# Performance work log

Measured on AMD Instinct MI355X. Metric: run time of the kernel, lower is better.

## Reference

```python
import jax, jax.numpy as jnp
import numpy as np

SEQ_LEN, HORIZON = 12, 12
B, N, DIN, DOUT, U = 16, 512, 2, 1, 64
NEG = -1e9


def _gat(x, W, a, b, mask):
    # x: (B, N, F_in); W: (F_in, G); a: (2, G); mask: (N, N) bool
    h = jnp.einsum('bnf,fg->bng', x, W)            # (B, N, G)
    src = jnp.einsum('bng,g->bn', h, a[0])         # (B, N)
    dst = jnp.einsum('bng,g->bn', h, a[1])         # (B, N)
    e = jax.nn.leaky_relu(src[:, :, None] + dst[:, None, :], 0.2)  # (B, N, N)
    e = jnp.where(mask[None], e, NEG)
    alpha = jax.nn.softmax(e, axis=-1)
    return jnp.einsum('bij,bjg->big', alpha, h) + b


def _cell(x, h_prev, W_ru, a_ru, b_ru, W_c, a_c, b_c, mask):
    # graph-attention GRU cell: x (B,N,Din), h_prev (B,N,U)
    xh = jnp.concatenate([x, h_prev], axis=-1)
    ru = jax.nn.sigmoid(_gat(xh, W_ru, a_ru, b_ru, mask))   # (B,N,2U)
    r, u = jnp.split(ru, 2, axis=-1)
    xc = jnp.concatenate([x, r * h_prev], axis=-1)
    c = jnp.tanh(_gat(xc, W_c, a_c, b_c, mask))
    return u * h_prev + (1.0 - u) * c


def setup_inputs() -> dict:
    key = jax.random.key(0)
    ks = jax.random.split(key, 16)
    s = 0.05
    inp = {
        'inputs': jax.random.normal(ks[0], (SEQ_LEN, B, N * DIN), jnp.float32),
        'adj': jax.random.uniform(ks[1], (N, N), jnp.float32),
        # encoder GAGRU cell (input_dim = DIN)
        'enc_W_ru': jax.random.normal(ks[2], (DIN + U, 2 * U), jnp.float32) * s,
        'enc_a_ru': jax.random.normal(ks[3], (2, 2 * U), jnp.float32) * s,
        'enc_b_ru': jnp.zeros((2 * U,), jnp.float32),
        'enc_W_c': jax.random.normal(ks[4], (DIN + U, U), jnp.float32) * s,
        'enc_a_c': jax.random.normal(ks[5], (2, U), jnp.float32) * s,
        'enc_b_c': jnp.zeros((U,), jnp.float32),
        # decoder GAGRU cell (input_dim = DOUT)
        'dec_W_ru': jax.random.normal(ks[6], (DOUT + U, 2 * U), jnp.float32) * s,
        'dec_a_ru': jax.random.normal(ks[7], (2, 2 * U), jnp.float32) * s,
        'dec_b_ru': jnp.zeros((2 * U,), jnp.float32),
        'dec_W_c': jax.random.normal(ks[8], (DOUT + U, U), jnp.float32) * s,
        'dec_a_c': jax.random.normal(ks[9], (2, U), jnp.float32) * s,
        'dec_b_c': jnp.zeros((U,), jnp.float32),
        # projection Linear(rnn_units -> output_dim)
        'proj_W': jax.random.normal(ks[10], (U, DOUT), jnp.float32) * s,
        'proj_b': jnp.zeros((DOUT,), jnp.float32),
    }
    return inp


def reference(inputs, adj, enc_W_ru, enc_a_ru, enc_b_ru, enc_W_c, enc_a_c, enc_b_c,
              dec_W_ru, dec_a_ru, dec_b_ru, dec_W_c, dec_a_c, dec_b_c, proj_W, proj_b):
    mask = (adj > 0.9) | jnp.eye(N, dtype=bool)
    x_seq = inputs.reshape(SEQ_LEN, B, N, DIN)

    # ---- encoder: scan GAGRU cell over seq_len ----
    def enc_step(h, x_t):
        h_new = _cell(x_t, h, enc_W_ru, enc_a_ru, enc_b_ru, enc_W_c, enc_a_c, enc_b_c, mask)
        return h_new, None

    h0 = jnp.zeros((B, N, U), inputs.dtype)
    h_enc, _ = jax.lax.scan(enc_step, h0, x_seq)

    def dec_step(carry, _):
        y_prev, h = carry
        h_new = _cell(y_prev, h, dec_W_ru, dec_a_ru, dec_b_ru, dec_W_c, dec_a_c, dec_b_c, mask)
        y = jnp.einsum('bnu,ud->bnd', h_new, proj_W) + proj_b  # (B, N, DOUT)
        return (y, h_new), y

    go = jnp.zeros((B, N, DOUT), inputs.dtype)
    _, outputs = jax.lax.scan(dec_step, (go, h_enc), None, length=HORIZON)
    return outputs  # (horizon, B, N, DOUT)
```

## Files before the change

kernel.cpp:

```cpp
#include <hip/hip_runtime.h>
#include <math.h>


#define NB 16
#define NN 512
#define NU 64
#define CAP 128
#define WPB 8

#define AS1 __attribute__((address_space(1)))
#define AS3 __attribute__((address_space(3)))

__device__ __forceinline__ void ld_lds16(float* lds_uniform, const float* g_perlane) {
#if __has_builtin(__builtin_amdgcn_global_load_lds)
  __builtin_amdgcn_global_load_lds((const AS1 unsigned int*)g_perlane,
                                   (AS3 unsigned int*)lds_uniform, 16, 0, 0);
#else
  int lane = threadIdx.x & 63;
  *(float4*)(lds_uniform + lane * 4) = *(const float4*)(g_perlane);
#endif
}

__device__ __forceinline__ void stage_weights(float* sW, const float* W, int TB,
                                              int w, int lane) {
  for (int c = w; c * 1024 < TB; c += WPB) {
    int off = c * 1024 + lane * 16;
    if (off < TB)
      ld_lds16((float*)((char*)sW + c * 1024), (const float*)((const char*)W + off));
  }
}

__device__ __forceinline__ float rlane(float v, int l) {
  return __int_as_float(__builtin_amdgcn_readlane(__float_as_int(v), l));
}
__device__ __forceinline__ int rlane_i(int v, int l) {
  return __builtin_amdgcn_readlane(v, l);
}
__device__ __forceinline__ float wave_max(float v) {
  #pragma unroll
  for (int s = 1; s < 64; s <<= 1) v = fmaxf(v, __shfl_xor(v, s));
  return v;
}
__device__ __forceinline__ float wave_sum(float v) {
  #pragma unroll
  for (int s = 1; s < 64; s <<= 1) v += __shfl_xor(v, s);
  return v;
}
__device__ __forceinline__ void wave_sum2(float& x, float& y) {
  #pragma unroll
  for (int s = 1; s < 64; s <<= 1) { x += __shfl_xor(x, s); y += __shfl_xor(y, s); }
}
__device__ __forceinline__ float fast_rcp(float x) {
#if __has_builtin(__builtin_amdgcn_rcpf)
  return __builtin_amdgcn_rcpf(x);
#else
  return 1.0f / x;
#endif
}
__device__ __forceinline__ float sigmoid_f(float x) {
  return fast_rcp(1.0f + __expf(-x));
}
__device__ __forceinline__ float tanh_f(float x) {
  return 1.0f - 2.0f * fast_rcp(__expf(2.0f * x) + 1.0f);
}

__global__ __launch_bounds__(64) void k_adj(const float* __restrict__ adj,
                                            int* __restrict__ cnt,
                                            int* __restrict__ idx) {
  int i = blockIdx.x;
  int l = threadIdx.x;
  int base = 0;
  #pragma unroll
  for (int c = 0; c < 8; ++c) {
    int j = c * 64 + l;
    bool pred = (adj[i * NN + j] > 0.9f) || (j == i);
    unsigned long long m = __ballot(pred);
    int pos = base + __popcll(m & ((1ull << l) - 1ull));
    if (pred && pos < CAP) idx[i * CAP + pos] = j;
    base += __popcll(m);
  }
  int total = base > CAP ? CAP : base;
  for (int p = total + l; p < CAP; p += 64) idx[i * CAP + p] = i;
  if (l == 0) cnt[i] = total;
}

template <int DIN>
__global__ __launch_bounds__(512, 6) void k_phaseB(
    const int* __restrict__ cnt, const int* __restrict__ idx,
    const float* __restrict__ h_ru, const float* __restrict__ src_ru,
    const float* __restrict__ dst_ru, const float* __restrict__ b_ru,
    const float* __restrict__ h, const float* __restrict__ x_ptr,
    const float* __restrict__ W_c, const float* __restrict__ a_c,
    float* __restrict__ h_c, float* __restrict__ src_c,
    float* __restrict__ dst_c, float* __restrict__ u_buf) {
  constexpr int TB = (DIN + NU) * NU * 4;
  __shared__ float sW[(DIN + NU) * NU];
  __shared__ float sh[WPB * NU];
  const int tid = threadIdx.x;
  const int w = tid >> 6, lane = tid & 63;

  stage_weights(sW, W_c, TB, w, lane);

  const int b = blockIdx.x >> 6;
  const int i = ((blockIdx.x & 63) << 3) | w;
  const int base_bi = (b << 9) + i;
  const float* __restrict__ hrb = h_ru + ((size_t)b << 16);
  const float* __restrict__ drb = dst_ru + (b << 9);

  const int c_ = cnt[i];
  const float si = src_ru[base_bi];
  const int j0 = idx[(i << 7) + lane];
  const int j1 = idx[(i << 7) + 64 + lane];
  float e0 = -1e30f, e1 = -1e30f;
  if (lane < c_)      { float t = si + drb[j0]; e0 = t >= 0.f ? t : 0.2f * t; }
  if (lane + 64 < c_) { float t = si + drb[j1]; e1 = t >= 0.f ? t : 0.2f * t; }
  float m = wave_max(fmaxf(e0, e1));
  float p0 = (lane < c_) ? __expf(e0 - m) : 0.f;
  float p1 = (lane + 64 < c_) ? __expf(e1 - m) : 0.f;
  float inv = fast_rcp(wave_sum(p0 + p1));
  p0 *= inv; p1 *= inv;

  const int g0 = lane << 1;
  float A0 = 0.f, A1 = 0.f, B0 = 0.f, B1 = 0.f;
  const int cc = (c_ + 15) & ~15;
  for (int base = 0; base < cc; base += 16) {
    float2 hv[16];
    #pragma unroll
    for (int q = 0; q < 16; ++q) {
      int jj = base + q;
      int sl = jj & 63;
      int j = (jj < 64) ? rlane_i(j0, sl) : rlane_i(j1, sl);
      hv[q] = *(const float2*)(hrb + (j << 7) + g0);
    }
    #pragma unroll
    for (int q = 0; q < 16; ++q) {
      int jj = base + q;
      int sl = jj & 63;
      float pv = (jj < 64) ? rlane(p0, sl) : rlane(p1, sl);
      if (q & 1) { B0 = fmaf(pv, hv[q].x, B0); B1 = fmaf(pv, hv[q].y, B1); }
      else       { A0 = fmaf(pv, hv[q].x, A0); A1 = fmaf(pv, hv[q].y, A1); }
    }
  }
  A0 += B0; A1 += B1;

  const float2 br = *(const float2*)(b_ru + g0);
  const float ru0 = sigmoid_f(A0 + br.x);
  const float ru1 = sigmoid_f(A1 + br.y);

  if (lane < 32) {
    float2 hh = *(const float2*)(h + ((size_t)base_bi << 6) + g0);
    *(float2*)&sh[(w << 6) + g0] = make_float2(ru0 * hh.x, ru1 * hh.y);
  } else {
    *(float2*)(u_buf + ((size_t)base_bi << 6) + (g0 - 64)) = make_float2(ru0, ru1);
  }

  __syncthreads();

  float acc;
  if (DIN == 2) {
    float2 xv = *(const float2*)(x_ptr + ((size_t)base_bi << 1));
    acc = xv.x * sW[lane];
    acc = fmaf(xv.y, sW[NU + lane], acc);
  } else {
    acc = x_ptr[base_bi] * sW[lane];
  }
  const float* __restrict__ sWh = sW + DIN * NU;
  const float* shw = sh + (w << 6);
  #pragma unroll
  for (int f2 = 0; f2 < 32; ++f2) {
    float2 rv = *(const float2*)(shw + 2 * f2);
    acc = fmaf(rv.x, sWh[(2 * f2) * NU + lane], acc);
    acc = fmaf(rv.y, sWh[(2 * f2 + 1) * NU + lane], acc);
  }
  h_c[((size_t)base_bi << 6) + lane] = acc;
  float s0 = acc * a_c[lane];
  float s1 = acc * a_c[NU + lane];
  wave_sum2(s0, s1);
  if (lane == 0) { src_c[base_bi] = s0; dst_c[base_bi] = s1; }
}

template <int UPD, int DIN_NEXT, int XMODE, int OUT>
__global__ __launch_bounds__(512, 6) void k_phaseA(
    const int* __restrict__ cnt, const int* __restrict__ idx,
    const float* __restrict__ h_c, const float* __restrict__ src_c,
    const float* __restrict__ dst_c, const float* __restrict__ b_c,
    const float* __restrict__ u_buf, float* __restrict__ h,
    const float* __restrict__ proj_W, const float* __restrict__ proj_b,
    float* __restrict__ out_slice, float* __restrict__ y_buf,
    const float* __restrict__ x_ptr,
    const float* __restrict__ W_ru, const float* __restrict__ a_ru,
    float* __restrict__ h_ru, float* __restrict__ src_ru,
    float* __restrict__ dst_ru) {
  constexpr int SWN = (DIN_NEXT > 0) ? (DIN_NEXT + NU) * 128 : 1;
  constexpr int TB = (DIN_NEXT > 0) ? SWN * 4 : 0;
  __shared__ float sW[SWN];
  __shared__ float sh[WPB * NU];
  const int tid = threadIdx.x;
  const int w = tid >> 6, lane = tid & 63;

  if (DIN_NEXT > 0) stage_weights(sW, W_ru, TB, w, lane);

  const int b = blockIdx.x >> 6;
  const int i = ((blockIdx.x & 63) << 3) | w;
  const int base_bi = (b << 9) + i;

  float hn = 0.f;
  if (UPD) {
    const float* __restrict__ hcb = h_c + ((size_t)b << 15);
    const float* __restrict__ dcb = dst_c + (b << 9);
    const int c_ = cnt[i];
    const float si = src_c[base_bi];
    const int j0 = idx[(i << 7) + lane];
    const int j1 = idx[(i << 7) + 64 + lane];
    float e0 = -1e30f, e1 = -1e30f;
    if (lane < c_)      { float t = si + dcb[j0]; e0 = t >= 0.f ? t : 0.2f * t; }
    if (lane + 64 < c_) { float t = si + dcb[j1]; e1 = t >= 0.f ? t : 0.2f * t; }
    float m = wave_max(fmaxf(e0, e1));
    float p0 = (lane < c_) ? __expf(e0 - m) : 0.f;
    float p1 = (lane + 64 < c_) ? __expf(e1 - m) : 0.f;
    float inv = fast_rcp(wave_sum(p0 + p1));
    p0 *= inv; p1 *= inv;

    float A = 0.f, Bacc = 0.f;
    const int cc = (c_ + 15) & ~15;
    for (int base = 0; base < cc; base += 16) {
      float hv[16];
      #pragma unroll
      for (int q = 0; q < 16; ++q) {
        int jj = base + q;
        int sl = jj & 63;
        int j = (jj < 64) ? rlane_i(j0, sl) : rlane_i(j1, sl);
        hv[q] = hcb[(j << 6) + lane];
      }
      #pragma unroll
      for (int q = 0; q < 16; ++q) {
        int jj = base + q;
        int sl = jj & 63;
        float pv = (jj < 64) ? rlane(p0, sl) : rlane(p1, sl);
        if (q & 1) Bacc = fmaf(pv, hv[q], Bacc);
        else       A = fmaf(pv, hv[q], A);
      }
    }
    A += Bacc;
    const float cc_ = tanh_f(A + b_c[lane]);
    const float u = u_buf[((size_t)base_bi << 6) + lane];
    const float ho = h[((size_t)base_bi << 6) + lane];
    hn = fmaf(u, ho - cc_, cc_);
  }
  h[((size_t)base_bi << 6) + lane] = hn;
  sh[(w << 6) + lane] = hn;

  float y = 0.f;
  if (OUT) {
    float t = wave_sum(hn * proj_W[lane]);
    y = t + proj_b[0];
    if (lane == 0) { out_slice[base_bi] = y; y_buf[base_bi] = y; }
  }

  if (DIN_NEXT > 0) {
    __syncthreads();
    const int g0 = lane << 1;
    float a0, a1;
    if (XMODE == 0) {
      if (DIN_NEXT == 2) {
        float2 xv = *(const float2*)(x_ptr + ((size_t)base_bi << 1));
        a0 = xv.x * sW[g0];
        a1 = xv.x * sW[g0 + 1];
        a0 = fmaf(xv.y, sW[128 + g0], a0);
        a1 = fmaf(xv.y, sW[128 + g0 + 1], a1);
      } else {
        float xv = x_ptr[base_bi];
        a0 = xv * sW[g0]; a1 = xv * sW[g0 + 1];
      }
    } else if (XMODE == 2) {
      a0 = y * sW[g0]; a1 = y * sW[g0 + 1];
    } else {
      a0 = 0.f; a1 = 0.f;
    }
    const float* __restrict__ sWh = sW + DIN_NEXT * 128;
    const float* shw = sh + (w << 6);
    #pragma unroll
    for (int f2 = 0; f2 < 32; ++f2) {
      float2 hp = *(const float2*)(shw + 2 * f2);
      float2 w0 = *(const float2*)(sWh + (2 * f2) * 128 + g0);
      float2 w1 = *(const float2*)(sWh + (2 * f2 + 1) * 128 + g0);
      a0 = fmaf(hp.x, w0.x, a0); a1 = fmaf(hp.x, w0.y, a1);
      a0 = fmaf(hp.y, w1.x, a0); a1 = fmaf(hp.y, w1.y, a1);
    }
    *(float2*)(h_ru + ((size_t)base_bi << 7) + g0) = make_float2(a0, a1);
    const float2 ar0 = *(const float2*)(a_ru + g0);
    const float2 ar1 = *(const float2*)(a_ru + 128 + g0);
    float s0 = a0 * ar0.x + a1 * ar0.y;
    float s1 = a0 * ar1.x + a1 * ar1.y;
    wave_sum2(s0, s1);
    if (lane == 0) { src_ru[base_bi] = s0; dst_ru[base_bi] = s1; }
  }
}

extern "C" void kernel_launch(void* const* d_in, const int* in_sizes, int n_in,
                              void* d_out, int out_size, void* d_ws, size_t ws_size,
                              hipStream_t stream) {
  (void)in_sizes; (void)n_in; (void)out_size; (void)ws_size;
  const float* inputs   = (const float*)d_in[0];
  const float* adj      = (const float*)d_in[1];
  const float* enc_W_ru = (const float*)d_in[2];
  const float* enc_a_ru = (const float*)d_in[3];
  const float* enc_b_ru = (const float*)d_in[4];
  const float* enc_W_c  = (const float*)d_in[5];
  const float* enc_a_c  = (const float*)d_in[6];
  const float* enc_b_c  = (const float*)d_in[7];
  const float* dec_W_ru = (const float*)d_in[8];
  const float* dec_a_ru = (const float*)d_in[9];
  const float* dec_b_ru = (const float*)d_in[10];
  const float* dec_W_c  = (const float*)d_in[11];
  const float* dec_a_c  = (const float*)d_in[12];
  const float* dec_b_c  = (const float*)d_in[13];
  const float* proj_W   = (const float*)d_in[14];
  const float* proj_b   = (const float*)d_in[15];
  float* out = (float*)d_out;

  char* ws = (char*)d_ws;
  int*   cnt    = (int*)ws;
  int*   idx    = (int*)(ws + 2048);
  float* h      = (float*)(ws + 264192);
  float* h_ru   = (float*)(ws + 2361344);
  float* src_ru = (float*)(ws + 6555648);
  float* dst_ru = (float*)(ws + 6588416);
  float* h_c    = (float*)(ws + 6621184);
  float* src_c  = (float*)(ws + 8718336);
  float* dst_c  = (float*)(ws + 8751104);
  float* u_buf  = (float*)(ws + 8783872);
  float* y_buf  = (float*)(ws + 10881024);

  hipMemsetAsync(y_buf, 0, NB * NN * sizeof(float), stream);
  k_adj<<<NN, 64, 0, stream>>>(adj, cnt, idx);

  const int GRID = (NB * NN) / WPB;

  k_phaseA<0, 2, 0, 0><<<GRID, 512, 0, stream>>>(cnt, idx, h_c, src_c, dst_c,
      enc_b_c, u_buf, h, proj_W, proj_b, nullptr, y_buf,
      inputs, enc_W_ru, enc_a_ru, h_ru, src_ru, dst_ru);

  for (int t = 0; t < 12; ++t) {
    k_phaseB<2><<<GRID, 512, 0, stream>>>(cnt, idx, h_ru, src_ru, dst_ru, enc_b_ru,
        h, inputs + (size_t)t * NB * NN * 2, enc_W_c, enc_a_c,
        h_c, src_c, dst_c, u_buf);
    if (t < 11)
      k_phaseA<1, 2, 0, 0><<<GRID, 512, 0, stream>>>(cnt, idx, h_c, src_c, dst_c,
          enc_b_c, u_buf, h, proj_W, proj_b, nullptr, y_buf,
          inputs + (size_t)(t + 1) * NB * NN * 2, enc_W_ru, enc_a_ru,
          h_ru, src_ru, dst_ru);
    else
      k_phaseA<1, 1, 1, 0><<<GRID, 512, 0, stream>>>(cnt, idx, h_c, src_c, dst_c,
          enc_b_c, u_buf, h, proj_W, proj_b, nullptr, y_buf,
          nullptr, dec_W_ru, dec_a_ru, h_ru, src_ru, dst_ru);
  }

  for (int k = 0; k < 12; ++k) {
    k_phaseB<1><<<GRID, 512, 0, stream>>>(cnt, idx, h_ru, src_ru, dst_ru, dec_b_ru,
        h, y_buf, dec_W_c, dec_a_c, h_c, src_c, dst_c, u_buf);
    if (k < 11)
      k_phaseA<1, 1, 2, 1><<<GRID, 512, 0, stream>>>(cnt, idx, h_c, src_c, dst_c,
          dec_b_c, u_buf, h, proj_W, proj_b, out + (size_t)k * NB * NN, y_buf,
          nullptr, dec_W_ru, dec_a_ru, h_ru, src_ru, dst_ru);
    else
      k_phaseA<1, 0, 1, 1><<<GRID, 512, 0, stream>>>(cnt, idx, h_c, src_c, dst_c,
          dec_b_c, u_buf, h, proj_W, proj_b, out + (size_t)k * NB * NN, y_buf,
          nullptr, dec_W_ru, dec_a_ru, h_ru, src_ru, dst_ru);
  }
}
```

Before: 905.3 us.

## Process two batches per wave to reuse neighbor indices and staged weights

Each wave now handles the same node for two batch elements, sharing the adjacency index loads, the softmax setup, and the LDS-staged weight reads across both. The grid is halved, so the per-block weight staging into LDS is amortized over twice the work. The trade-off is higher register pressure from the doubled accumulators and gather buffers (the gather unroll drops from 16 to 8). There are also fewer blocks, which lowers the available parallelism.

```diff
diff --git a/kernel.cpp b/kernel.cpp
--- a/kernel.cpp
+++ b/kernel.cpp
@@ -36,19 +36,23 @@
 __device__ __forceinline__ int rlane_i(int v, int l) {
   return __builtin_amdgcn_readlane(v, l);
 }
-__device__ __forceinline__ float wave_max(float v) {
+__device__ __forceinline__ void wave_max2(float& x, float& y) {
   #pragma unroll
-  for (int s = 1; s < 64; s <<= 1) v = fmaxf(v, __shfl_xor(v, s));
-  return v;
-}
-__device__ __forceinline__ float wave_sum(float v) {
-  #pragma unroll
-  for (int s = 1; s < 64; s <<= 1) v += __shfl_xor(v, s);
-  return v;
+  for (int s = 1; s < 64; s <<= 1) {
+    x = fmaxf(x, __shfl_xor(x, s));
+    y = fmaxf(y, __shfl_xor(y, s));
+  }
 }
 __device__ __forceinline__ void wave_sum2(float& x, float& y) {
   #pragma unroll
   for (int s = 1; s < 64; s <<= 1) { x += __shfl_xor(x, s); y += __shfl_xor(y, s); }
+}
+__device__ __forceinline__ void wave_sum4(float& a, float& b, float& c, float& d) {
+  #pragma unroll
+  for (int s = 1; s < 64; s <<= 1) {
+    a += __shfl_xor(a, s); b += __shfl_xor(b, s);
+    c += __shfl_xor(c, s); d += __shfl_xor(d, s);
+  }
 }
 __device__ __forceinline__ float fast_rcp(float x) {
 #if __has_builtin(__builtin_amdgcn_rcpf)
@@ -62,6 +66,11 @@
 }
 __device__ __forceinline__ float tanh_f(float x) {
   return 1.0f - 2.0f * fast_rcp(__expf(2.0f * x) + 1.0f);
+}
+
+__device__ __forceinline__ void decode_block(int bx, int w, int& b0, int& i) {
+  b0 = (bx & 7) << 1;
+  i = (((bx >> 3)) << 3) | w;
 }
 
 __global__ __launch_bounds__(64) void k_adj(const float* __restrict__ adj,
@@ -95,88 +104,112 @@
     float* __restrict__ dst_c, float* __restrict__ u_buf) {
   constexpr int TB = (DIN + NU) * NU * 4;
   __shared__ float sW[(DIN + NU) * NU];
-  __shared__ float sh[WPB * NU];
+  __shared__ float sh[WPB * 2 * NU];
   const int tid = threadIdx.x;
   const int w = tid >> 6, lane = tid & 63;
 
   stage_weights(sW, W_c, TB, w, lane);
 
-  const int b = blockIdx.x >> 6;
-  const int i = ((blockIdx.x & 63) << 3) | w;
-  const int base_bi = (b << 9) + i;
-  const float* __restrict__ hrb = h_ru + ((size_t)b << 16);
-  const float* __restrict__ drb = dst_ru + (b << 9);
+  int b0, i;
+  decode_block(blockIdx.x, w, b0, i);
+  const int bi0 = (b0 << 9) + i, bi1 = bi0 + NN;
+  const float* __restrict__ hrb0 = h_ru + ((size_t)b0 << 16);
+  const float* __restrict__ drb0 = dst_ru + (b0 << 9);
 
   const int c_ = cnt[i];
-  const float si = src_ru[base_bi];
   const int j0 = idx[(i << 7) + lane];
   const int j1 = idx[(i << 7) + 64 + lane];
-  float e0 = -1e30f, e1 = -1e30f;
-  if (lane < c_)      { float t = si + drb[j0]; e0 = t >= 0.f ? t : 0.2f * t; }
-  if (lane + 64 < c_) { float t = si + drb[j1]; e1 = t >= 0.f ? t : 0.2f * t; }
-  float m = wave_max(fmaxf(e0, e1));
-  float p0 = (lane < c_) ? __expf(e0 - m) : 0.f;
-  float p1 = (lane + 64 < c_) ? __expf(e1 - m) : 0.f;
-  float inv = fast_rcp(wave_sum(p0 + p1));
-  p0 *= inv; p1 *= inv;
+  const float si0 = src_ru[bi0], si1 = src_ru[bi1];
+  float e00 = -1e30f, e01 = -1e30f, e10 = -1e30f, e11 = -1e30f;
+  if (lane < c_) {
+    float t0 = si0 + drb0[j0];      e00 = t0 >= 0.f ? t0 : 0.2f * t0;
+    float t1 = si1 + drb0[NN + j0]; e10 = t1 >= 0.f ? t1 : 0.2f * t1;
+  }
+  if (lane + 64 < c_) {
+    float t0 = si0 + drb0[j1];      e01 = t0 >= 0.f ? t0 : 0.2f * t0;
+    float t1 = si1 + drb0[NN + j1]; e11 = t1 >= 0.f ? t1 : 0.2f * t1;
+  }
+  float m0 = fmaxf(e00, e01), m1 = fmaxf(e10, e11);
+  wave_max2(m0, m1);
+  float p00 = (lane < c_)      ? __expf(e00 - m0) : 0.f;
+  float p01 = (lane + 64 < c_) ? __expf(e01 - m0) : 0.f;
+  float p10 = (lane < c_)      ? __expf(e10 - m1) : 0.f;
+  float p11 = (lane + 64 < c_) ? __expf(e11 - m1) : 0.f;
+  float s0 = p00 + p01, s1 = p10 + p11;
+  wave_sum2(s0, s1);
+  float inv0 = fast_rcp(s0), inv1 = fast_rcp(s1);
+  p00 *= inv0; p01 *= inv0; p10 *= inv1; p11 *= inv1;
 
   const int g0 = lane << 1;
-  float A0 = 0.f, A1 = 0.f, B0 = 0.f, B1 = 0.f;
-  const int cc = (c_ + 15) & ~15;
-  for (int base = 0; base < cc; base += 16) {
-    float2 hv[16];
+  float A00 = 0.f, A01 = 0.f, A10 = 0.f, A11 = 0.f;
+  const int ccn = (c_ + 7) & ~7;
+  for (int base = 0; base < ccn; base += 8) {
+    float2 hv0[8], hv1[8];
     #pragma unroll
-    for (int q = 0; q < 16; ++q) {
-      int jj = base + q;
-      int sl = jj & 63;
+    for (int q = 0; q < 8; ++q) {
+      int jj = base + q; int sl = jj & 63;
       int j = (jj < 64) ? rlane_i(j0, sl) : rlane_i(j1, sl);
-      hv[q] = *(const float2*)(hrb + (j << 7) + g0);
+      const float* p = hrb0 + (j << 7) + g0;
+      hv0[q] = *(const float2*)p;
+      hv1[q] = *(const float2*)(p + (1 << 16));
     }
     #pragma unroll
-    for (int q = 0; q < 16; ++q) {
-      int jj = base + q;
-      int sl = jj & 63;
-      float pv = (jj < 64) ? rlane(p0, sl) : rlane(p1, sl);
-      if (q & 1) { B0 = fmaf(pv, hv[q].x, B0); B1 = fmaf(pv, hv[q].y, B1); }
-      else       { A0 = fmaf(pv, hv[q].x, A0); A1 = fmaf(pv, hv[q].y, A1); }
-    }
-  }
-  A0 += B0; A1 += B1;
+    for (int q = 0; q < 8; ++q) {
+      int jj = base + q; int sl = jj & 63;
+      float pv0 = (jj < 64) ? rlane(p00, sl) : rlane(p01, sl);
+      float pv1 = (jj < 64) ? rlane(p10, sl) : rlane(p11, sl);
+      A00 = fmaf(pv0, hv0[q].x, A00); A01 = fmaf(pv0, hv0[q].y, A01);
+      A10 = fmaf(pv1, hv1[q].x, A10); A11 = fmaf(pv1, hv1[q].y, A11);
+    }
+  }
 
   const float2 br = *(const float2*)(b_ru + g0);
-  const float ru0 = sigmoid_f(A0 + br.x);
-  const float ru1 = sigmoid_f(A1 + br.y);
+  const float ru00 = sigmoid_f(A00 + br.x), ru01 = sigmoid_f(A01 + br.y);
+  const float ru10 = sigmoid_f(A10 + br.x), ru11 = sigmoid_f(A11 + br.y);
 
   if (lane < 32) {
-    float2 hh = *(const float2*)(h + ((size_t)base_bi << 6) + g0);
-    *(float2*)&sh[(w << 6) + g0] = make_float2(ru0 * hh.x, ru1 * hh.y);
+    float2 hh0 = *(const float2*)(h + ((size_t)bi0 << 6) + g0);
+    float2 hh1 = *(const float2*)(h + ((size_t)bi1 << 6) + g0);
+    *(float2*)&sh[(w << 7) + g0]      = make_float2(ru00 * hh0.x, ru01 * hh0.y);
+    *(float2*)&sh[(w << 7) + 64 + g0] = make_float2(ru10 * hh1.x, ru11 * hh1.y);
   } else {
-    *(float2*)(u_buf + ((size_t)base_bi << 6) + (g0 - 64)) = make_float2(ru0, ru1);
+    *(float2*)(u_buf + ((size_t)bi0 << 6) + (g0 - 64)) = make_float2(ru00, ru01);
+    *(float2*)(u_buf + ((size_t)bi1 << 6) + (g0 - 64)) = make_float2(ru10, ru11);
   }
 
   __syncthreads();
 
-  float acc;
+  float acc0, acc1;
   if (DIN == 2) {
-    float2 xv = *(const float2*)(x_ptr + ((size_t)base_bi << 1));
-    acc = xv.x * sW[lane];
-    acc = fmaf(xv.y, sW[NU + lane], acc);
+    float2 xv0 = *(const float2*)(x_ptr + ((size_t)bi0 << 1));
+    float2 xv1 = *(const float2*)(x_ptr + ((size_t)bi1 << 1));
+    acc0 = xv0.x * sW[lane]; acc0 = fmaf(xv0.y, sW[NU + lane], acc0);
+    acc1 = xv1.x * sW[lane]; acc1 = fmaf(xv1.y, sW[NU + lane], acc1);
   } else {
-    acc = x_ptr[base_bi] * sW[lane];
+    acc0 = x_ptr[bi0] * sW[lane];
+    acc1 = x_ptr[bi1] * sW[lane];
   }
   const float* __restrict__ sWh = sW + DIN * NU;
-  const float* shw = sh + (w << 6);
+  const float* shw0 = sh + (w << 7);
+  const float* shw1 = shw0 + 64;
   #pragma unroll
   for (int f2 = 0; f2 < 32; ++f2) {
-    float2 rv = *(const float2*)(shw + 2 * f2);
-    acc = fmaf(rv.x, sWh[(2 * f2) * NU + lane], acc);
-    acc = fmaf(rv.y, sWh[(2 * f2 + 1) * NU + lane], acc);
-  }
-  h_c[((size_t)base_bi << 6) + lane] = acc;
-  float s0 = acc * a_c[lane];
-  float s1 = acc * a_c[NU + lane];
-  wave_sum2(s0, s1);
-  if (lane == 0) { src_c[base_bi] = s0; dst_c[base_bi] = s1; }
+    float2 rv0 = *(const float2*)(shw0 + 2 * f2);
+    float2 rv1 = *(const float2*)(shw1 + 2 * f2);
+    float w0 = sWh[(2 * f2) * NU + lane];
+    float w1 = sWh[(2 * f2 + 1) * NU + lane];
+    acc0 = fmaf(rv0.x, w0, acc0); acc0 = fmaf(rv0.y, w1, acc0);
+    acc1 = fmaf(rv1.x, w0, acc1); acc1 = fmaf(rv1.y, w1, acc1);
+  }
+  h_c[((size_t)bi0 << 6) + lane] = acc0;
+  h_c[((size_t)bi1 << 6) + lane] = acc1;
+  float s00 = acc0 * a_c[lane], s01 = acc0 * a_c[NU + lane];
+  float s10 = acc1 * a_c[lane], s11 = acc1 * a_c[NU + lane];
+  wave_sum4(s00, s01, s10, s11);
+  if (lane == 0) {
+    src_c[bi0] = s00; dst_c[bi0] = s01;
+    src_c[bi1] = s10; dst_c[bi1] = s11;
+  }
 }
 
 template <int UPD, int DIN_NEXT, int XMODE, int OUT>
@@ -194,106 +227,143 @@
   constexpr int SWN = (DIN_NEXT > 0) ? (DIN_NEXT + NU) * 128 : 1;
   constexpr int TB = (DIN_NEXT > 0) ? SWN * 4 : 0;
   __shared__ float sW[SWN];
-  __shared__ float sh[WPB * NU];
+  __shared__ float sh[WPB * 2 * NU];
   const int tid = threadIdx.x;
   const int w = tid >> 6, lane = tid & 63;
 
   if (DIN_NEXT > 0) stage_weights(sW, W_ru, TB, w, lane);
 
-  const int b = blockIdx.x >> 6;
-  const int i = ((blockIdx.x & 63) << 3) | w;
-  const int base_bi = (b << 9) + i;
-
-  float hn = 0.f;
+  int b0, i;
+  decode_block(blockIdx.x, w, b0, i);
+  const int bi0 = (b0 << 9) + i, bi1 = bi0 + NN;
+
+  float hn0 = 0.f, hn1 = 0.f;
   if (UPD) {
-    const float* __restrict__ hcb = h_c + ((size_t)b << 15);
-    const float* __restrict__ dcb = dst_c + (b << 9);
+    const float* __restrict__ hcb0 = h_c + ((size_t)b0 << 15);
+    const float* __restrict__ dcb0 = dst_c + (b0 << 9);
     const int c_ = cnt[i];
-    const float si = src_c[base_bi];
     const int j0 = idx[(i << 7) + lane];
     const int j1 = idx[(i << 7) + 64 + lane];
-    float e0 = -1e30f, e1 = -1e30f;
-    if (lane < c_)      { float t = si + dcb[j0]; e0 = t >= 0.f ? t : 0.2f * t; }
-    if (lane + 64 < c_) { float t = si + dcb[j1]; e1 = t >= 0.f ? t : 0.2f * t; }
-    float m = wave_max(fmaxf(e0, e1));
-    float p0 = (lane < c_) ? __expf(e0 - m) : 0.f;
-    float p1 = (lane + 64 < c_) ? __expf(e1 - m) : 0.f;
-    float inv = fast_rcp(wave_sum(p0 + p1));
-    p0 *= inv; p1 *= inv;
-
-    float A = 0.f, Bacc = 0.f;
-    const int cc = (c_ + 15) & ~15;
-    for (int base = 0; base < cc; base += 16) {
-      float hv[16];
+    const float si0 = src_c[bi0], si1 = src_c[bi1];
+    float e00 = -1e30f, e01 = -1e30f, e10 = -1e30f, e11 = -1e30f;
+    if (lane < c_) {
+      float t0 = si0 + dcb0[j0];      e00 = t0 >= 0.f ? t0 : 0.2f * t0;
+      float t1 = si1 + dcb0[NN + j0]; e10 = t1 >= 0.f ? t1 : 0.2f * t1;
+    }
+    if (lane + 64 < c_) {
+      float t0 = si0 + dcb0[j1];      e01 = t0 >= 0.f ? t0 : 0.2f * t0;
+      float t1 = si1 + dcb0[NN + j1]; e11 = t1 >= 0.f ? t1 : 0.2f * t1;
+    }
+    float m0 = fmaxf(e00, e01), m1 = fmaxf(e10, e11);
+    wave_max2(m0, m1);
+    float p00 = (lane < c_)      ? __expf(e00 - m0) : 0.f;
+    float p01 = (lane + 64 < c_) ? __expf(e01 - m0) : 0.f;
+    float p10 = (lane < c_)      ? __expf(e10 - m1) : 0.f;
+    float p11 = (lane + 64 < c_) ? __expf(e11 - m1) : 0.f;
+    float s0 = p00 + p01, s1 = p10 + p11;
+    wave_sum2(s0, s1);
+    float inv0 = fast_rcp(s0), inv1 = fast_rcp(s1);
+    p00 *= inv0; p01 *= inv0; p10 *= inv1; p11 *= inv1;
+
+    float A0 = 0.f, B0 = 0.f, A1 = 0.f, B1 = 0.f;
+    const int ccn = (c_ + 7) & ~7;
+    for (int base = 0; base < ccn; base += 8) {
+      float hv0[8], hv1[8];
       #pragma unroll
-      for (int q = 0; q < 16; ++q) {
-        int jj = base + q;
-        int sl = jj & 63;
+      for (int q = 0; q < 8; ++q) {
+        int jj = base + q; int sl = jj & 63;
         int j = (jj < 64) ? rlane_i(j0, sl) : rlane_i(j1, sl);
-        hv[q] = hcb[(j << 6) + lane];
+        const float* p = hcb0 + (j << 6) + lane;
+        hv0[q] = *p;
+        hv1[q] = *(p + (1 << 15));
       }
       #pragma unroll
-      for (int q = 0; q < 16; ++q) {
-        int jj = base + q;
-        int sl = jj & 63;
-        float pv = (jj < 64) ? rlane(p0, sl) : rlane(p1, sl);
-        if (q & 1) Bacc = fmaf(pv, hv[q], Bacc);
-        else       A = fmaf(pv, hv[q], A);
+      for (int q = 0; q < 8; ++q) {
+        int jj = base + q; int sl = jj & 63;
+        float pv0 = (jj < 64) ? rlane(p00, sl) : rlane(p01, sl);
+        float pv1 = (jj < 64) ? rlane(p10, sl) : rlane(p11, sl);
+        if (q & 1) { B0 = fmaf(pv0, hv0[q], B0); B1 = fmaf(pv1, hv1[q], B1); }
+        else       { A0 = fmaf(pv0, hv0[q], A0); A1 = fmaf(pv1, hv1[q], A1); }
       }
     }
-    A += Bacc;
-    const float cc_ = tanh_f(A + b_c[lane]);
-    const float u = u_buf[((size_t)base_bi << 6) + lane];
-    const float ho = h[((size_t)base_bi << 6) + lane];
-    hn = fmaf(u, ho - cc_, cc_);
-  }
-  h[((size_t)base_bi << 6) + lane] = hn;
-  sh[(w << 6) + lane] = hn;
-
-  float y = 0.f;
+    A0 += B0; A1 += B1;
+    const float bc = b_c[lane];
+    const float cc0 = tanh_f(A0 + bc), cc1 = tanh_f(A1 + bc);
+    const float u0 = u_buf[((size_t)bi0 << 6) + lane];
+    const float u1 = u_buf[((size_t)bi1 << 6) + lane];
+    const float ho0 = h[((size_t)bi0 << 6) + lane];
+    const float ho1 = h[((size_t)bi1 << 6) + lane];
+    hn0 = fmaf(u0, ho0 - cc0, cc0);
+    hn1 = fmaf(u1, ho1 - cc1, cc1);
+  }
+  h[((size_t)bi0 << 6) + lane] = hn0;
+  h[((size_t)bi1 << 6) + lane] = hn1;
+  sh[(w << 7) + lane] = hn0;
+  sh[(w << 7) + 64 + lane] = hn1;
+
+  float y0 = 0.f, y1 = 0.f;
   if (OUT) {
-    float t = wave_sum(hn * proj_W[lane]);
-    y = t + proj_b[0];
-    if (lane == 0) { out_slice[base_bi] = y; y_buf[base_bi] = y; }
+    float t0 = hn0 * proj_W[lane];
+    float t1 = hn1 * proj_W[lane];
+    wave_sum2(t0, t1);
+    y0 = t0 + proj_b[0];
+    y1 = t1 + proj_b[0];
+    if (lane == 0) {
+      out_slice[bi0] = y0; y_buf[bi0] = y0;
+      out_slice[bi1] = y1; y_buf[bi1] = y1;
+    }
   }
 
   if (DIN_NEXT > 0) {
     __syncthreads();
     const int g0 = lane << 1;
-    float a0, a1;
+    float a00, a01, a10, a11;
     if (XMODE == 0) {
       if (DIN_NEXT == 2) {
-        float2 xv = *(const float2*)(x_ptr + ((size_t)base_bi << 1));
-        a0 = xv.x * sW[g0];
-        a1 = xv.x * sW[g0 + 1];
-        a0 = fmaf(xv.y, sW[128 + g0], a0);
-        a1 = fmaf(xv.y, sW[128 + g0 + 1], a1);
+        float2 xv0 = *(const float2*)(x_ptr + ((size_t)bi0 << 1));
+        float2 xv1 = *(const float2*)(x_ptr + ((size_t)bi1 << 1));
+        a00 = xv0.x * sW[g0]; a01 = xv0.x * sW[g0 + 1];
+        a00 = fmaf(xv0.y, sW[128 + g0], a00); a01 = fmaf(xv0.y, sW[128 + g0 + 1], a01);
+        a10 = xv1.x * sW[g0]; a11 = xv1.x * sW[g0 + 1];
+        a10 = fmaf(xv1.y, sW[128 + g0], a10); a11 = fmaf(xv1.y, sW[128 + g0 + 1], a11);
       } else {
-        float xv = x_ptr[base_bi];
-        a0 = xv * sW[g0]; a1 = xv * sW[g0 + 1];
+        float xv0 = x_ptr[bi0], xv1 = x_ptr[bi1];
+        a00 = xv0 * sW[g0]; a01 = xv0 * sW[g0 + 1];
+        a10 = xv1 * sW[g0]; a11 = xv1 * sW[g0 + 1];
       }
     } else if (XMODE == 2) {
-      a0 = y * sW[g0]; a1 = y * sW[g0 + 1];
+      a00 = y0 * sW[g0]; a01 = y0 * sW[g0 + 1];
+      a10 = y1 * sW[g0]; a11 = y1 * sW[g0 + 1];
     } else {
-      a0 = 0.f; a1 = 0.f;
+      a00 = 0.f; a01 = 0.f; a10 = 0.f; a11 = 0.f;
     }
     const float* __restrict__ sWh = sW + DIN_NEXT * 128;
-    const float* shw = sh + (w << 6);
+    const float* shw0 = sh + (w << 7);
+    const float* shw1 = shw0 + 64;
     #pragma unroll
     for (int f2 = 0; f2 < 32; ++f2) {
-      float2 hp = *(const float2*)(shw + 2 * f2);
+      float2 hp0 = *(const float2*)(shw0 + 2 * f2);
+      float2 hp1 = *(const float2*)(shw1 + 2 * f2);
       float2 w0 = *(const float2*)(sWh + (2 * f2) * 128 + g0);
       float2 w1 = *(const float2*)(sWh + (2 * f2 + 1) * 128 + g0);
-      a0 = fmaf(hp.x, w0.x, a0); a1 = fmaf(hp.x, w0.y, a1);
-      a0 = fmaf(hp.y, w1.x, a0); a1 = fmaf(hp.y, w1.y, a1);
-    }
-    *(float2*)(h_ru + ((size_t)base_bi << 7) + g0) = make_float2(a0, a1);
+      a00 = fmaf(hp0.x, w0.x, a00); a01 = fmaf(hp0.x, w0.y, a01);
+      a00 = fmaf(hp0.y, w1.x, a00); a01 = fmaf(hp0.y, w1.y, a01);
+      a10 = fmaf(hp1.x, w0.x, a10); a11 = fmaf(hp1.x, w0.y, a11);
+      a10 = fmaf(hp1.y, w1.x, a10); a11 = fmaf(hp1.y, w1.y, a11);
+    }
+    *(float2*)(h_ru + ((size_t)bi0 << 7) + g0) = make_float2(a00, a01);
+    *(float2*)(h_ru + ((size_t)bi1 << 7) + g0) = make_float2(a10, a11);
     const float2 ar0 = *(const float2*)(a_ru + g0);
     const float2 ar1 = *(const float2*)(a_ru + 128 + g0);
-    float s0 = a0 * ar0.x + a1 * ar0.y;
-    float s1 = a0 * ar1.x + a1 * ar1.y;
-    wave_sum2(s0, s1);
-    if (lane == 0) { src_ru[base_bi] = s0; dst_ru[base_bi] = s1; }
+    float s00 = a00 * ar0.x + a01 * ar0.y;
+    float s01 = a00 * ar1.x + a01 * ar1.y;
+    float s10 = a10 * ar0.x + a11 * ar0.y;
+    float s11 = a10 * ar1.x + a11 * ar1.y;
+    wave_sum4(s00, s01, s10, s11);
+    if (lane == 0) {
+      src_ru[bi0] = s00; dst_ru[bi0] = s01;
+      src_ru[bi1] = s10; dst_ru[bi1] = s11;
+    }
   }
 }
 
@@ -335,7 +405,7 @@
   hipMemsetAsync(y_buf, 0, NB * NN * sizeof(float), stream);
   k_adj<<<NN, 64, 0, stream>>>(adj, cnt, idx);
 
-  const int GRID = (NB * NN) / WPB;
+  const int GRID = (NB * NN) / (WPB * 2);
 
   k_phaseA<0, 2, 0, 0><<<GRID, 512, 0, stream>>>(cnt, idx, h_c, src_c, dst_c,
       enc_b_c, u_buf, h, proj_W, proj_b, nullptr, y_buf,
```

Result: slower. 976.2 us (+7.8%).
